# Optimization experiments

Measured on AMD Instinct MI355X. Metric: run time of the kernel, lower is better.

## Reference

```python
import jax, jax.numpy as jnp
import numpy as np

C = 256
NH, NL, NP_ = 8, 3, 4
HD = C // NH
NLAYERS = 6


def sine_pos(H, W, num_feats=128, temperature=10000.0, eps=1e-6):
    # mmdet SinePositionalEncoding with normalize=True and an all-zero padding mask:
    # cumsum of ones -> (i+1), normalized by last element (H or W) * 2*pi.
    scale = 2.0 * np.pi
    y = (jnp.arange(1, H + 1, dtype=jnp.float32) / (H + eps)) * scale
    x = (jnp.arange(1, W + 1, dtype=jnp.float32) / (W + eps)) * scale
    d = jnp.arange(num_feats, dtype=jnp.float32)
    dim_t = temperature ** (2.0 * jnp.floor(d / 2.0) / num_feats)

    def interleave(p):  # p: (n, num_feats) -> sin on even dims, cos on odd dims, interleaved
        return jnp.stack([jnp.sin(p[:, 0::2]), jnp.cos(p[:, 1::2])], axis=-1).reshape(p.shape[0], -1)

    py = interleave(y[:, None] / dim_t)  # (H, num_feats)
    px = interleave(x[:, None] / dim_t)  # (W, num_feats)
    pos = jnp.concatenate([jnp.broadcast_to(py[:, None, :], (H, W, num_feats)),
                           jnp.broadcast_to(px[None, :, :], (H, W, num_feats))], axis=-1)
    return pos.reshape(H * W, 2 * num_feats)


def ref_points(H, W):
    # normalized pixel centers, (x, y) order, shape (H*W, 2)
    ry = (jnp.arange(H, dtype=jnp.float32) + 0.5) / H
    rx = (jnp.arange(W, dtype=jnp.float32) + 0.5) / W
    gy, gx = jnp.meshgrid(ry, rx, indexing='ij')
    return jnp.stack([gx.ravel(), gy.ravel()], axis=-1)


def ln(x, w, b, eps=1e-5):
    m = x.mean(-1, keepdims=True)
    v = x.var(-1, keepdims=True)
    return (x - m) / jnp.sqrt(v + eps) * w + b


def gnorm(x, w, b, groups=32, eps=1e-5):
    B, Ch, H, W = x.shape
    xg = x.reshape(B, groups, Ch // groups, H, W)
    m = xg.mean((2, 3, 4), keepdims=True)
    v = xg.var((2, 3, 4), keepdims=True)
    xg = (xg - m) / jnp.sqrt(v + eps)
    return xg.reshape(B, Ch, H, W) * w[None, :, None, None] + b[None, :, None, None]


def conv3x3(x, w):
    return jax.lax.conv_general_dilated(x, w, (1, 1), 'SAME',
                                        dimension_numbers=('NCHW', 'OIHW', 'NCHW'))


def ms_deform(value, shapes, loc, aw):
    # value (B,S,NH,HD); loc (B,L,NH,NL,NP,2) normalized [0,1]; aw (B,L,NH,NL,NP)
    # Matches F.grid_sample(..., align_corners=False, padding_mode='zeros').
    B, S, nH, hd = value.shape
    Lq, nP = loc.shape[1], loc.shape[4]
    out = jnp.zeros((B, Lq, nH, hd), value.dtype)
    start = 0
    for lvl, (H, W) in enumerate(shapes):
        v = value[:, start:start + H * W].transpose(0, 2, 1, 3)  # (B,nH,HW,hd)
        start += H * W
        l = loc[:, :, :, lvl]                 # (B,Lq,nH,nP,2)
        px = l[..., 0] * W - 0.5
        py = l[..., 1] * H - 0.5
        x0 = jnp.floor(px); y0 = jnp.floor(py)
        lx = px - x0; ly = py - y0
        x0i = x0.astype(jnp.int32); y0i = y0.astype(jnp.int32)

        def tw(w_):  # (B,Lq,nH,nP) -> (B,nH,Lq*nP,1)
            return w_.transpose(0, 2, 1, 3).reshape(B, nH, Lq * nP, 1)

        def gather(xi, yi):
            valid = ((xi >= 0) & (xi < W) & (yi >= 0) & (yi < H)).astype(value.dtype)
            idx = jnp.clip(yi, 0, H - 1) * W + jnp.clip(xi, 0, W - 1)
            idx = idx.transpose(0, 2, 1, 3).reshape(B, nH, Lq * nP)
            g = jnp.take_along_axis(v, idx[..., None], axis=2)  # (B,nH,Lq*nP,hd)
            return g * tw(valid)

        samp = (gather(x0i, y0i) * tw((1 - lx) * (1 - ly))
                + gather(x0i + 1, y0i) * tw(lx * (1 - ly))
                + gather(x0i, y0i + 1) * tw((1 - lx) * ly)
                + gather(x0i + 1, y0i + 1) * tw(lx * ly))
        samp = samp.reshape(B, nH, Lq, nP, hd)
        out = out + jnp.einsum('bqhp,bhqpd->bqhd', aw[:, :, :, lvl], samp)
    return out.reshape(B, Lq, nH * hd)


def _forward(feat0, feat1, feat2, in0_w, in0_b, in1_w, in1_b, in2_w, in2_b,
             off_w, off_b, aw_w, aw_b, vp_w, vp_b, op_w, op_b,
             n1_w, n1_b, ff1_w, ff1_b, ff2_w, ff2_b, n2_w, n2_b,
             fn_w, fn_b, lat_w, lat_b, out_w, gnw, gnb):
    feats = [feat0, feat1, feat2]
    in_ws = [in0_w, in1_w, in2_w]; in_bs = [in0_b, in1_b, in2_b]
    B = feat0.shape[0]
    mlvl = [jnp.einsum('oi,bihw->bohw', w, f) + b[None, :, None, None]
            for f, w, b in zip(feats, in_ws, in_bs)]
    shapes = [(f.shape[2], f.shape[3]) for f in mlvl]
    src = jnp.concatenate([f.reshape(B, C, -1).transpose(0, 2, 1) for f in mlvl], axis=1)  # (B,L,C)
    pos = jnp.concatenate([sine_pos(H, W) for (H, W) in shapes], axis=0)[None]  # (1,L,C)
    ref = jnp.concatenate([ref_points(H, W) for (H, W) in shapes], axis=0)      # (L,2)
    L = ref.shape[0]
    ref = jnp.broadcast_to(ref[None, :, None, :], (B, L, NL, 2))
    norm = jnp.array([[w_, h_] for (h_, w_) in shapes], dtype=src.dtype)  # (NL,2) = (W,H)
    for i in range(NLAYERS):
        q = src + pos
        off = (q @ off_w[i].T + off_b[i]).reshape(B, L, NH, NL, NP_, 2)
        aw = jax.nn.softmax((q @ aw_w[i].T + aw_b[i]).reshape(B, L, NH, NL * NP_), axis=-1)
        aw = aw.reshape(B, L, NH, NL, NP_)
        value = (src @ vp_w[i].T + vp_b[i]).reshape(B, L, NH, HD)
        loc = ref[:, :, None, :, None, :] + off / norm[None, None, None, :, None, :]
        attn = ms_deform(value, shapes, loc, aw) @ op_w[i].T + op_b[i]
        src = ln(src + attn, n1_w[i], n1_b[i])
        ff = jax.nn.relu(src @ ff1_w[i].T + ff1_b[i]) @ ff2_w[i].T + ff2_b[i]
        src = ln(src + ff, n2_w[i], n2_b[i])
    src = ln(src, fn_w, fn_b)
    mems, s = [], 0
    for (H, W) in shapes:
        mems.append(src[:, s:s + H * W].transpose(0, 2, 1).reshape(B, C, H, W))
        s += H * W
    mf = jnp.einsum('oi,bihw->bohw', lat_w, mems[0]) + lat_b[None, :, None, None]
    for i in range(3):
        mf = jax.nn.relu(gnorm(conv3x3(mf, out_w[i]), gnw[i], gnb[i]))
    return (mf, mems[0], mems[1], mems[2])


def setup_inputs():
    ks = iter(jax.random.split(jax.random.key(0), 64))

    def rn(shape, s=0.02):
        return jax.random.normal(next(ks), shape, dtype=jnp.float32) * s

    return dict(
        feat0=rn((1, 256, 64, 64), 1.0),
        feat1=rn((1, 512, 32, 32), 1.0),
        feat2=rn((1, 1024, 16, 16), 1.0),
        in0_w=rn((256, 256)), in0_b=rn((256,)),
        in1_w=rn((256, 512)), in1_b=rn((256,)),
        in2_w=rn((256, 1024)), in2_b=rn((256,)),
        off_w=rn((6, 192, 256), 0.002), off_b=rn((6, 192), 0.5),
        aw_w=rn((6, 96, 256)), aw_b=jnp.zeros((6, 96), jnp.float32),
        vp_w=rn((6, 256, 256)), vp_b=rn((6, 256)),
        op_w=rn((6, 256, 256)), op_b=rn((6, 256)),
        n1_w=jnp.ones((6, 256), jnp.float32), n1_b=jnp.zeros((6, 256), jnp.float32),
        ff1_w=rn((6, 1024, 256)), ff1_b=rn((6, 1024)),
        ff2_w=rn((6, 256, 1024)), ff2_b=rn((6, 256)),
        n2_w=jnp.ones((6, 256), jnp.float32), n2_b=jnp.zeros((6, 256), jnp.float32),
        fn_w=jnp.ones((256,), jnp.float32), fn_b=jnp.zeros((256,), jnp.float32),
        lat_w=rn((256, 256)), lat_b=rn((256,)),
        out_w=rn((3, 256, 256, 3, 3)),
        gnw=jnp.ones((3, 256), jnp.float32), gnb=jnp.zeros((3, 256), jnp.float32),
    )


def reference(feat0, feat1, feat2, in0_w, in0_b, in1_w, in1_b, in2_w, in2_b,
              off_w, off_b, aw_w, aw_b, vp_w, vp_b, op_w, op_b,
              n1_w, n1_b, ff1_w, ff1_b, ff2_w, ff2_b, n2_w, n2_b,
              fn_w, fn_b, lat_w, lat_b, out_w, gnw, gnb):
    return _forward(feat0, feat1, feat2, in0_w, in0_b, in1_w, in1_b, in2_w, in2_b,
                    off_w, off_b, aw_w, aw_b, vp_w, vp_b, op_w, op_b,
                    n1_w, n1_b, ff1_w, ff1_b, ff2_w, ff2_b, n2_w, n2_b,
                    fn_w, fn_b, lat_w, lat_b, out_w, gnw, gnb)
```

## Files before the change

kernel.cpp:

```cpp
#include <hip/hip_runtime.h>
#include <math.h>

#define LTOT 5376

typedef __attribute__((ext_vector_type(8))) __bf16 bf16x8;
typedef __attribute__((ext_vector_type(4))) float f32x4;
typedef __attribute__((ext_vector_type(8))) unsigned short us8;
typedef __attribute__((ext_vector_type(4))) unsigned short us4;

static __device__ __forceinline__ float4 ld4(const float* p) { return *(const float4*)p; }

static __device__ __forceinline__ unsigned short f2bf(float f) {
    unsigned int u = __float_as_uint(f);
    return (unsigned short)((u + 0x7fffu + ((u >> 16) & 1u)) >> 16);
}
static __device__ __forceinline__ float bf2f(unsigned short s) {
    return __uint_as_float(((unsigned int)s) << 16);
}

static __device__ __forceinline__ void gl16(const unsigned short* g, unsigned short* l) {
    __builtin_amdgcn_global_load_lds(
        (const __attribute__((address_space(1))) unsigned int*)g,
        (__attribute__((address_space(3))) unsigned int*)l, 16, 0, 0);
}

__device__ __forceinline__ void gemm_core(
    const unsigned short* __restrict__ A,
    const unsigned short* __restrict__ B,
    const float* __restrict__ bias,
    float* __restrict__ C1, unsigned short* __restrict__ C2,
    const float* __restrict__ posf, unsigned short* __restrict__ qb,
    unsigned short* As, unsigned short* Bs,
    int m0, int mo0, int n0, int N, int K, int omode, int relu)
{
    const int tid  = threadIdx.x;
    const int wave = tid >> 6;
    const int lane = tid & 63;
    const int wm   = (wave >> 1) * 32;
    const int wn   = (wave & 1) * 32;
    const int fr   = lane & 15;
    const int ko   = lane >> 4;

    const int q0 = tid, q1 = tid + 256;
    const int r0 = q0 >> 3, c0v = (q0 & 7) ^ (r0 & 7);
    const int r1 = q1 >> 3, c1v = (q1 & 7) ^ (r1 & 7);
    const unsigned short* a0 = A + (size_t)(m0 + r0) * K + (c0v << 3);
    const unsigned short* a1 = A + (size_t)(m0 + r1) * K + (c1v << 3);
    int bn0 = n0 + r0; if (bn0 > N - 1) bn0 = N - 1;
    int bn1 = n0 + r1; if (bn1 > N - 1) bn1 = N - 1;
    const unsigned short* b0 = B + (size_t)bn0 * K + (c0v << 3);
    const unsigned short* b1 = B + (size_t)bn1 * K + (c1v << 3);
    const int wb = wave << 9;

    f32x4 acc[2][2] = {};
    const int nt = K >> 6;

    auto stage = [&](int buf, int t) {
        const int kof = t << 6;
        gl16(a0 + kof, As + buf * 4096 + wb);
        gl16(a1 + kof, As + buf * 4096 + 2048 + wb);
        gl16(b0 + kof, Bs + buf * 4096 + wb);
        gl16(b1 + kof, Bs + buf * 4096 + 2048 + wb);
    };

    stage(0, 0);
    stage(1, 1);
    asm volatile("s_waitcnt vmcnt(4)" ::: "memory");
    __builtin_amdgcn_s_barrier();
    __builtin_amdgcn_sched_barrier(0);

    for (int t = 0; t < nt; t++) {
        if (t + 2 < nt) stage((t + 2) % 3, t + 2);
        const unsigned short* Ab = As + (t % 3) * 4096;
        const unsigned short* Bb = Bs + (t % 3) * 4096;
        #pragma unroll
        for (int sub = 0; sub < 2; sub++) {
            bf16x8 af[2], bfr[2];
            const int kk = (sub << 2) + ko;
            #pragma unroll
            for (int i = 0; i < 2; i++) {
                int r = wm + i * 16 + fr;
                af[i] = *(const bf16x8*)&Ab[(r << 6) + ((kk ^ (r & 7)) << 3)];
                int c = wn + i * 16 + fr;
                bfr[i] = *(const bf16x8*)&Bb[(c << 6) + ((kk ^ (c & 7)) << 3)];
            }
            #pragma unroll
            for (int i = 0; i < 2; i++)
                #pragma unroll
                for (int j = 0; j < 2; j++)
                    acc[i][j] = __builtin_amdgcn_mfma_f32_16x16x32_bf16(af[i], bfr[j], acc[i][j], 0, 0, 0);
        }
        if (t + 1 < nt) {
            if (t + 2 < nt) asm volatile("s_waitcnt vmcnt(4) lgkmcnt(0)" ::: "memory");
            else            asm volatile("s_waitcnt vmcnt(0) lgkmcnt(0)" ::: "memory");
            __builtin_amdgcn_s_barrier();
            __builtin_amdgcn_sched_barrier(0);
        }
    }

    #pragma unroll
    for (int j = 0; j < 2; j++) {
        int col = n0 + wn + j * 16 + fr;
        if (col >= N) continue;
        float cb = bias[col];
        #pragma unroll
        for (int i = 0; i < 2; i++) {
            #pragma unroll
            for (int r = 0; r < 4; r++) {
                int row = mo0 + wm + i * 16 + ko * 4 + r;
                float v = acc[i][j][r] + cb;
                if (relu) v = fmaxf(v, 0.f);
                size_t off = (size_t)row * N + col;
                if (omode == 0)      C1[off] = v;
                else if (omode == 1) C2[off] = f2bf(v);
                else if (omode == 2) { C1[off] = v; C2[off] = f2bf(v); }
                else { C1[off] = v; C2[off] = f2bf(v); qb[off] = f2bf(v + posf[off]); }
            }
        }
    }
}

__global__ __launch_bounds__(256) void bgemm_k(
    const unsigned short* __restrict__ A, const unsigned short* __restrict__ B,
    const float* __restrict__ bias, float* __restrict__ C1, unsigned short* __restrict__ C2,
    int N, int K, int omode, int relu)
{
    __shared__ unsigned short As[3 * 4096], Bs[3 * 4096];
    int m = blockIdx.y * 64;
    gemm_core(A, B, bias, C1, C2, nullptr, nullptr, As, Bs, m, m, blockIdx.x * 64, N, K, omode, relu);
}

__global__ __launch_bounds__(256) void oavp_k(
    const unsigned short* __restrict__ qbb, const unsigned short* __restrict__ woa,
    const float* __restrict__ boa, float* __restrict__ oab,
    const unsigned short* __restrict__ srcb, const unsigned short* __restrict__ wvp,
    const float* __restrict__ bvp, unsigned short* __restrict__ valb)
{
    __shared__ unsigned short As[3 * 4096], Bs[3 * 4096];
    const int bx = blockIdx.x;
    const int m = blockIdx.y * 64;
    if (bx < 5)
        gemm_core(qbb,  woa, boa, oab, nullptr, nullptr, nullptr, As, Bs, m, m, bx * 64, 288, 256, 0, 0);
    else
        gemm_core(srcb, wvp, bvp, nullptr, valb, nullptr, nullptr, As, Bs, m, m, (bx - 5) * 64, 256, 256, 1, 0);
}

__global__ __launch_bounds__(256) void inproj_k(
    const unsigned short* __restrict__ fT0, const unsigned short* __restrict__ w0, const float* __restrict__ b0,
    const unsigned short* __restrict__ fT1, const unsigned short* __restrict__ w1, const float* __restrict__ b1,
    const unsigned short* __restrict__ fT2, const unsigned short* __restrict__ w2, const float* __restrict__ b2,
    float* __restrict__ src, unsigned short* __restrict__ srcb,
    const float* __restrict__ posf, unsigned short* __restrict__ qbb)
{
    __shared__ unsigned short As[3 * 4096], Bs[3 * 4096];
    const int by = blockIdx.y;
    const int n0 = blockIdx.x * 64;
    if (by < 64)
        gemm_core(fT0, w0, b0, src, srcb, posf, qbb, As, Bs, by * 64, by * 64, n0, 256, 256, 3, 0);
    else if (by < 80)
        gemm_core(fT1, w1, b1, src, srcb, posf, qbb, As, Bs, (by - 64) * 64, 4096 + (by - 64) * 64, n0, 256, 512, 3, 0);
    else
        gemm_core(fT2, w2, b2, src, srcb, posf, qbb, As, Bs, (by - 80) * 64, 5120 + (by - 80) * 64, n0, 256, 1024, 3, 0);
}

__global__ __launch_bounds__(256) void setup_k(
    const float* __restrict__ off_w, const float* __restrict__ off_b,
    const float* __restrict__ aw_w,  const float* __restrict__ aw_b,
    unsigned short* __restrict__ w_oa, float* __restrict__ b_oa,
    const float* __restrict__ out_w, unsigned short* __restrict__ wcb,
    const float* __restrict__ s0, const float* __restrict__ s1,
    const float* __restrict__ s2, const float* __restrict__ s3,
    const float* __restrict__ s4, const float* __restrict__ s5,
    const float* __restrict__ s6, const float* __restrict__ s7,
    unsigned short* __restrict__ dcvt,
    float* __restrict__ pos,
    const float* __restrict__ f0, const float* __restrict__ f1, const float* __restrict__ f2,
    unsigned short* __restrict__ d0, unsigned short* __restrict__ d1, unsigned short* __restrict__ d2)
{
    const int bid = blockIdx.x;
    const int tid = threadIdx.x;
    if (bid < 1728) {
        int idx = bid * 256 + tid;
        int i = idx / 73728;
        int r = idx - i * 73728;
        int n = r >> 8;
        int k = r & 255;
        float v = (n < 192) ? off_w[((size_t)i * 192 + n) * 256 + k]
                            : aw_w[((size_t)i * 96 + (n - 192)) * 256 + k];
        w_oa[idx] = f2bf(v);
        if (k == 0)
            b_oa[i * 288 + n] = (n < 192) ? off_b[i * 192 + n] : aw_b[i * 96 + (n - 192)];
    } else if (bid < 8640) {
        int idx = (bid - 1728) * 256 + tid;
        int c   = idx / 589824;
        int r   = idx - c * 589824;
        int icc = r / 73728;
        int r2  = r - icc * 73728;
        int oc  = r2 / 288;
        int r3  = r2 - oc * 288;
        int tap = r3 >> 5;
        int sl  = r3 & 31;
        int ic  = icc * 32 + (((sl >> 3) ^ ((oc >> 1) & 3)) << 3) + (sl & 7);
        wcb[idx] = f2bf(out_w[(((size_t)(c * 256 + oc)) * 256 + ic) * 9 + tap]);
    } else if (bid < 12992) {
        int i = (bid - 8640) * 256 + tid;
        const float* s; int off;
        if      (i <   98304) { s = s0; off = 0; }
        else if (i <  196608) { s = s1; off = 98304; }
        else if (i <  589824) { s = s2; off = 196608; }
        else if (i <  983040) { s = s3; off = 589824; }
        else if (i <  999424) { s = s4; off = 983040; }
        else if (i < 1032192) { s = s5; off = 999424; }
        else if (i < 1097728) { s = s6; off = 1032192; }
        else                  { s = s7; off = 1097728; }
        float4 v = ld4(&s[(size_t)(i - off) << 2]);
        us4 r = { f2bf(v.x), f2bf(v.y), f2bf(v.z), f2bf(v.w) };
        *(us4*)&dcvt[(size_t)i << 2] = r;
    } else if (bid < 15680) {
        int idx = (bid - 12992) * 256 + tid;
        int l = idx >> 7;
        int pr = idx & 127;
        int half = pr >> 6;
        int j = pr & 63;
        int HW, sh, p;
        if (l < 4096)      { HW = 64; sh = 6; p = l; }
        else if (l < 5120) { HW = 32; sh = 5; p = l - 4096; }
        else               { HW = 16; sh = 4; p = l - 5120; }
        int y = p >> sh;
        int x = p & (HW - 1);
        float invT = exp2f((float)j * (-13.287712379549449f / 64.f));
        float coord = (half == 0) ? (float)(y + 1) : (float)(x + 1);
        float v = coord / ((float)HW + 1e-6f) * 6.283185307179586f;
        float arg = v * invT;
        size_t base = (size_t)l * 256 + half * 128 + (j << 1);
        pos[base]     = sinf(arg);
        pos[base + 1] = cosf(arg);
    } else {
        __shared__ float t[32][33];
        int b = bid - 15680;
        const float* src; unsigned short* dst; int Ci, P, bx, by;
        if (b < 1024)      { src = f0; dst = d0; Ci = 256;  P = 4096; bx = b & 127;        by = b >> 7; }
        else if (b < 1536) { src = f1; dst = d1; Ci = 512;  P = 1024; bx = (b - 1024) & 31; by = (b - 1024) >> 5; }
        else               { src = f2; dst = d2; Ci = 1024; P = 256;  bx = (b - 1536) & 7;  by = (b - 1536) >> 3; }
        int c0 = by * 32, p0 = bx * 32;
        int x = tid & 31, y = tid >> 5;
        for (int i = y; i < 32; i += 8)
            t[i][x] = src[(size_t)(c0 + i) * P + p0 + x];
        __syncthreads();
        for (int i = y; i < 32; i += 8)
            dst[(size_t)(p0 + i) * Ci + c0 + x] = f2bf(t[x][i]);
    }
}

__global__ __launch_bounds__(256) void msdef_k(
    const unsigned short* __restrict__ valb, const float* __restrict__ oab,
    unsigned short* __restrict__ out)
{
    __shared__ float sw[8 * 288];
    const int tid = threadIdx.x;
    const int bl = blockIdx.x;
    #pragma unroll
    for (int id = tid; id < 576; id += 256)
        ((float4*)sw)[id] = ((const float4*)(oab + (size_t)bl * 2304))[id];
    __syncthreads();

    const int p = tid >> 5;
    const int t = tid & 31;
    const int l = bl * 8 + p;
    const int h = t >> 2;
    const int co = (t & 3) << 3;
    const float* mo = sw + p * 288;

    float aw_r[12];
    {
        const float* sc = mo + 192 + h * 12;
        float mx = -1e30f;
        #pragma unroll
        for (int j = 0; j < 12; j++) { aw_r[j] = sc[j]; mx = fmaxf(mx, aw_r[j]); }
        float su = 0.f;
        #pragma unroll
        for (int j = 0; j < 12; j++) { aw_r[j] = expf(aw_r[j] - mx); su += aw_r[j]; }
        float inv = 1.f / su;
        #pragma unroll
        for (int j = 0; j < 12; j++) aw_r[j] *= inv;
    }

    float rx, ry;
    {
        int HW, sh, q;
        if (l < 4096)      { HW = 64; sh = 6; q = l; }
        else if (l < 5120) { HW = 32; sh = 5; q = l - 4096; }
        else               { HW = 16; sh = 4; q = l - 5120; }
        int y = q >> sh;
        int x = q & (HW - 1);
        rx = (x + 0.5f) / (float)HW;
        ry = (y + 0.5f) / (float)HW;
    }

    const int starts[3] = {0, 4096, 5120};
    const int dims[3]   = {64, 32, 16};
    float acc[8] = {};
    #pragma unroll
    for (int s = 0; s < 3; s++) {
        const int D = dims[s];
        const int st = starts[s];
        #pragma unroll
        for (int pt = 0; pt < 4; pt++) {
            float a  = aw_r[(s << 2) + pt];
            float px = rx * D + mo[h * 24 + (s << 3) + (pt << 1)]     - 0.5f;
            float py = ry * D + mo[h * 24 + (s << 3) + (pt << 1) + 1] - 0.5f;
            float x0f = floorf(px), y0f = floorf(py);
            float lx = px - x0f, ly = py - y0f;
            int x0 = (int)x0f, y0 = (int)y0f;
            float w00 = a * (1.f - lx) * (1.f - ly);
            float w10 = a * lx * (1.f - ly);
            float w01 = a * (1.f - lx) * ly;
            float w11 = a * lx * ly;
            #pragma unroll
            for (int cy = 0; cy < 2; cy++) {
                int yi = y0 + cy;
                if (yi < 0 || yi >= D) continue;
                #pragma unroll
                for (int cx = 0; cx < 2; cx++) {
                    int xi = x0 + cx;
                    if (xi < 0 || xi >= D) continue;
                    float w = cy ? (cx ? w11 : w01) : (cx ? w10 : w00);
                    us8 v = *(const us8*)&valb[((size_t)(st + yi * D + xi) << 8) + (h << 5) + co];
                    #pragma unroll
                    for (int e = 0; e < 8; e++)
                        acc[e] = fmaf(w, bf2f(v[e]), acc[e]);
                }
            }
        }
    }
    us8 r;
    #pragma unroll
    for (int e = 0; e < 8; e++) r[e] = f2bf(acc[e]);
    *(us8*)&out[((size_t)l << 8) + (h << 5) + co] = r;
}

template<bool HAS_POS>
__global__ __launch_bounds__(256) void ln_k(float* __restrict__ src, const float* __restrict__ add,
                                            const float* __restrict__ w, const float* __restrict__ b,
                                            unsigned short* __restrict__ outb,
                                            const float* __restrict__ posf,
                                            unsigned short* __restrict__ qbout)
{
    int row = blockIdx.x * 4 + (threadIdx.x >> 6);
    int lane = threadIdx.x & 63;
    size_t base = (size_t)row * 256 + (lane << 2);
    float4 x = ld4(&src[base]);
    float4 a = ld4(&add[base]);
    x.x += a.x; x.y += a.y; x.z += a.z; x.w += a.w;
    float s = x.x + x.y + x.z + x.w;
    #pragma unroll
    for (int o = 32; o > 0; o >>= 1) s += __shfl_xor(s, o, 64);
    float m = s * (1.f / 256.f);
    float d0 = x.x - m, d1 = x.y - m, d2 = x.z - m, d3 = x.w - m;
    float v = d0 * d0 + d1 * d1 + d2 * d2 + d3 * d3;
    #pragma unroll
    for (int o = 32; o > 0; o >>= 1) v += __shfl_xor(v, o, 64);
    float rs = rsqrtf(v * (1.f / 256.f) + 1e-5f);
    float4 wv = ld4(&w[lane << 2]);
    float4 bv = ld4(&b[lane << 2]);
    float4 o4;
    o4.x = d0 * rs * wv.x + bv.x;
    o4.y = d1 * rs * wv.y + bv.y;
    o4.z = d2 * rs * wv.z + bv.z;
    o4.w = d3 * rs * wv.w + bv.w;
    *(float4*)&src[base] = o4;
    us4 r = { f2bf(o4.x), f2bf(o4.y), f2bf(o4.z), f2bf(o4.w) };
    *(us4*)&outb[base] = r;
    if (HAS_POS) {
        float4 p4 = ld4(&posf[base]);
        us4 q = { f2bf(o4.x + p4.x), f2bf(o4.y + p4.y), f2bf(o4.z + p4.z), f2bf(o4.w + p4.w) };
        *(us4*)&qbout[base] = q;
    }
}

__global__ __launch_bounds__(256) void ln2fn_k(float* __restrict__ src, const float* __restrict__ add,
                                               const float* __restrict__ w2, const float* __restrict__ b2,
                                               const float* __restrict__ wf, const float* __restrict__ bf,
                                               unsigned short* __restrict__ outb)
{
    int row = blockIdx.x * 4 + (threadIdx.x >> 6);
    int lane = threadIdx.x & 63;
    size_t base = (size_t)row * 256 + (lane << 2);
    float4 x = ld4(&src[base]);
    float4 a = ld4(&add[base]);
    x.x += a.x; x.y += a.y; x.z += a.z; x.w += a.w;
    float s = x.x + x.y + x.z + x.w;
    #pragma unroll
    for (int o = 32; o > 0; o >>= 1) s += __shfl_xor(s, o, 64);
    float m = s * (1.f / 256.f);
    float d0 = x.x - m, d1 = x.y - m, d2 = x.z - m, d3 = x.w - m;
    float v = d0 * d0 + d1 * d1 + d2 * d2 + d3 * d3;
    #pragma unroll
    for (int o = 32; o > 0; o >>= 1) v += __shfl_xor(v, o, 64);
    float rs = rsqrtf(v * (1.f / 256.f) + 1e-5f);
    float4 wv = ld4(&w2[lane << 2]);
    float4 bv = ld4(&b2[lane << 2]);
    float4 o4;
    o4.x = d0 * rs * wv.x + bv.x;
    o4.y = d1 * rs * wv.y + bv.y;
    o4.z = d2 * rs * wv.z + bv.z;
    o4.w = d3 * rs * wv.w + bv.w;
    float s2 = o4.x + o4.y + o4.z + o4.w;
    #pragma unroll
    for (int o = 32; o > 0; o >>= 1) s2 += __shfl_xor(s2, o, 64);
    float m2 = s2 * (1.f / 256.f);
    float e0 = o4.x - m2, e1 = o4.y - m2, e2 = o4.z - m2, e3 = o4.w - m2;
    float v2 = e0 * e0 + e1 * e1 + e2 * e2 + e3 * e3;
    #pragma unroll
    for (int o = 32; o > 0; o >>= 1) v2 += __shfl_xor(v2, o, 64);
    float rs2 = rsqrtf(v2 * (1.f / 256.f) + 1e-5f);
    float4 wf4 = ld4(&wf[lane << 2]);
    float4 bf4 = ld4(&bf[lane << 2]);
    float4 o5;
    o5.x = e0 * rs2 * wf4.x + bf4.x;
    o5.y = e1 * rs2 * wf4.y + bf4.y;
    o5.z = e2 * rs2 * wf4.z + bf4.z;
    o5.w = e3 * rs2 * wf4.w + bf4.w;
    *(float4*)&src[base] = o5;
    us4 r = { f2bf(o5.x), f2bf(o5.y), f2bf(o5.z), f2bf(o5.w) };
    *(us4*)&outb[base] = r;
}

__global__ __launch_bounds__(256) void tail_k(
    const float* __restrict__ src, float* __restrict__ outb_,
    const unsigned short* __restrict__ srcb, const unsigned short* __restrict__ w_lat,
    const float* __restrict__ lat_b, unsigned short* __restrict__ latb)
{
    if (blockIdx.x < 1344) {
        __shared__ float t[32][33];
        int b = blockIdx.x;
        int bx = b % 168, cy = b / 168;
        const float* s; float* d; int HW, p0;
        if (bx < 128)      { s = src;           d = outb_;           HW = 4096; p0 = bx * 32; }
        else if (bx < 160) { s = src + 1048576; d = outb_ + 1048576; HW = 1024; p0 = (bx - 128) * 32; }
        else               { s = src + 1310720; d = outb_ + 1310720; HW = 256;  p0 = (bx - 160) * 32; }
        int c0 = cy * 32;
        int x = threadIdx.x & 31, y = threadIdx.x >> 5;
        for (int i = y; i < 32; i += 8)
            t[i][x] = s[(size_t)(p0 + i) * 256 + c0 + x];
        __syncthreads();
        for (int i = y; i < 32; i += 8)
            d[(size_t)(c0 + i) * HW + p0 + x] = t[x][i];
    } else {
        __shared__ unsigned short As[3 * 4096], Bs[3 * 4096];
        int b = blockIdx.x - 1344;
        int m = (b >> 2) * 64;
        gemm_core(srcb, w_lat, lat_b, nullptr, latb, nullptr, nullptr, As, Bs,
                  m, m, (b & 3) * 64, 256, 256, 1, 0);
    }
}

__global__ __launch_bounds__(256) void conv3b_k(const unsigned short* __restrict__ inb,
                                                const unsigned short* __restrict__ wcb,
                                                float* __restrict__ out)
{
    __shared__ __align__(16) unsigned char smem[25344];
    unsigned short* sIn = (unsigned short*)smem;
    unsigned short* sW  = (unsigned short*)(smem + 6912);
    float* sO = (float*)smem;

    const int tid = threadIdx.x;
    const int mb = blockIdx.x;
    const int y0 = (mb >> 2) << 2;
    const int x0 = (mb & 3) << 4;
    const int oc0 = blockIdx.y << 5;
    const int wave = tid >> 6, lane = tid & 63;
    const int wm = (wave >> 1) * 32;
    const int wn = (wave & 1) * 16;
    const int fr = lane & 15, ko = lane >> 4;

    f32x4 acc[2] = {};

    for (int icc = 0; icc < 8; icc++) {
        __syncthreads();
        #pragma unroll
        for (int id = tid; id < 432; id += 256) {
            int pxi = id >> 2, ch = id & 3;
            int r = pxi / 18, s = pxi - r * 18;
            int gy = y0 - 1 + r, gx = x0 - 1 + s;
            us8 v = {};
            if (gy >= 0 && gy < 64 && gx >= 0 && gx < 64)
                v = *(const us8*)&inb[((size_t)(gy * 64 + gx) << 8) + (icc << 5) + (ch << 3)];
            *(us8*)&sIn[(pxi << 5) + ((ch ^ ((s >> 1) & 3)) << 3)] = v;
        }
        const unsigned short* wsrc = wcb + (((size_t)icc * 256 + oc0) * 9 << 5);
        #pragma unroll
        for (int id = tid; id < 1152; id += 256)
            *(us8*)&sW[id << 3] = *(const us8*)&wsrc[id << 3];
        __syncthreads();

        #pragma unroll
        for (int tap = 0; tap < 9; tap++) {
            const int ky = tap / 3, kx = tap - ky * 3;
            bf16x8 a[2], b;
            #pragma unroll
            for (int i = 0; i < 2; i++) {
                int px = wm + i * 16 + fr;
                int r = (px >> 4) + ky;
                int s = (px & 15) + kx;
                a[i] = *(const bf16x8*)&sIn[(((r * 18 + s)) << 5) + ((ko ^ ((s >> 1) & 3)) << 3)];
            }
            {
                int oc = wn + fr;
                b = *(const bf16x8*)&sW[(((oc * 9) + tap) << 5) + ((ko ^ ((oc >> 1) & 3)) << 3)];
            }
            #pragma unroll
            for (int i = 0; i < 2; i++)
                acc[i] = __builtin_amdgcn_mfma_f32_16x16x32_bf16(a[i], b, acc[i], 0, 0, 0);
        }
    }

    __syncthreads();
    #pragma unroll
    for (int i = 0; i < 2; i++) {
        int oc = wn + fr;
        int pxb = wm + i * 16 + ko * 4;
        *(f32x4*)&sO[oc * 68 + pxb] = acc[i];
    }
    __syncthreads();
    {
        int oc_r = tid >> 3;
        int yy   = (tid >> 1) & 3;
        int xh   = (tid & 1) << 3;
        float* dst = &out[(size_t)(oc0 + oc_r) * 4096 + (y0 + yy) * 64 + x0 + xh];
        const float* srcl = &sO[oc_r * 68 + yy * 16 + xh];
        *(float4*)&dst[0] = *(const float4*)&srcl[0];
        *(float4*)&dst[4] = *(const float4*)&srcl[4];
    }
}

template<int OUT>
__global__ __launch_bounds__(1024) void gn_k(const float* __restrict__ x,
                                             const float* __restrict__ w, const float* __restrict__ b,
                                             unsigned short* __restrict__ ob, float* __restrict__ of)
{
    const int g = blockIdx.x;
    const float* p = x + (size_t)g * 32768;
    float s = 0.f, ss = 0.f;
    for (int i = threadIdx.x * 4; i < 32768; i += 4096) {
        float4 v = ld4(&p[i]);
        s  += v.x + v.y + v.z + v.w;
        ss += v.x * v.x + v.y * v.y + v.z * v.z + v.w * v.w;
    }
    #pragma unroll
    for (int o = 32; o > 0; o >>= 1) {
        s  += __shfl_xor(s, o, 64);
        ss += __shfl_xor(ss, o, 64);
    }
    __shared__ float rs[16], rss[16];
    int wid = threadIdx.x >> 6;
    if ((threadIdx.x & 63) == 0) { rs[wid] = s; rss[wid] = ss; }
    __syncthreads();
    float S = 0.f, SS = 0.f;
    #pragma unroll
    for (int k = 0; k < 16; k++) { S += rs[k]; SS += rss[k]; }
    float m = S * (1.f / 32768.f);
    float rstd = rsqrtf(SS * (1.f / 32768.f) - m * m + 1e-5f);

    for (int i = threadIdx.x; i < 8192; i += 1024) {
        int cl = i >> 10;
        int c = (g << 3) + cl;
        float sw = w[c], sb = b[c];
        float4 v = ld4(&p[(size_t)i << 2]);
        float r0 = fmaxf((v.x - m) * rstd * sw + sb, 0.f);
        float r1 = fmaxf((v.y - m) * rstd * sw + sb, 0.f);
        float r2 = fmaxf((v.z - m) * rstd * sw + sb, 0.f);
        float r3 = fmaxf((v.w - m) * rstd * sw + sb, 0.f);
        if (OUT == 0) {
            int px0 = (i & 1023) << 2;
            ob[(size_t)(px0 + 0) * 256 + c] = f2bf(r0);
            ob[(size_t)(px0 + 1) * 256 + c] = f2bf(r1);
            ob[(size_t)(px0 + 2) * 256 + c] = f2bf(r2);
            ob[(size_t)(px0 + 3) * 256 + c] = f2bf(r3);
        } else {
            float4 r = make_float4(r0, r1, r2, r3);
            *(float4*)&of[(size_t)g * 32768 + ((size_t)i << 2)] = r;
        }
    }
}

extern "C" void kernel_launch(void* const* d_in, const int* in_sizes, int n_in,
                              void* d_out, int out_size, void* d_ws, size_t ws_size,
                              hipStream_t stream)
{
    (void)in_sizes; (void)n_in; (void)out_size; (void)ws_size;
    const float* feat0 = (const float*)d_in[0];
    const float* feat1 = (const float*)d_in[1];
    const float* feat2 = (const float*)d_in[2];
    const float* in0_w = (const float*)d_in[3];
    const float* in0_b = (const float*)d_in[4];
    const float* in1_w = (const float*)d_in[5];
    const float* in1_b = (const float*)d_in[6];
    const float* in2_w = (const float*)d_in[7];
    const float* in2_b = (const float*)d_in[8];
    const float* off_w = (const float*)d_in[9];
    const float* off_b = (const float*)d_in[10];
    const float* aw_w  = (const float*)d_in[11];
    const float* aw_b  = (const float*)d_in[12];
    const float* vp_w  = (const float*)d_in[13];
    const float* vp_b  = (const float*)d_in[14];
    const float* op_w  = (const float*)d_in[15];
    const float* op_b  = (const float*)d_in[16];
    const float* n1_w  = (const float*)d_in[17];
    const float* n1_b  = (const float*)d_in[18];
    const float* ff1_w = (const float*)d_in[19];
    const float* ff1_b = (const float*)d_in[20];
    const float* ff2_w = (const float*)d_in[21];
    const float* ff2_b = (const float*)d_in[22];
    const float* n2_w  = (const float*)d_in[23];
    const float* n2_b  = (const float*)d_in[24];
    const float* fn_w  = (const float*)d_in[25];
    const float* fn_b  = (const float*)d_in[26];
    const float* lat_w = (const float*)d_in[27];
    const float* lat_b = (const float*)d_in[28];
    const float* out_w = (const float*)d_in[29];
    const float* gnw   = (const float*)d_in[30];
    const float* gnb   = (const float*)d_in[31];
    float* out = (float*)d_out;

    float* ws     = (float*)d_ws;
    float* src    = ws;
    float* pos    = src  + 1376256;
    float* tmp    = pos  + 1376256;
    float* valbuf = tmp  + 1376256;
    float* oab    = valbuf + 1376256;
    float* stats  = oab  + 1548288;
    float* boa    = stats + 64;
    float* pong   = pos;

    unsigned short* valb = (unsigned short*)valbuf;
    unsigned short* latb = (unsigned short*)(valbuf + 688128);

    unsigned short* ub = (unsigned short*)(boa + 1728);
    unsigned short* srcb  = ub; ub += 1376256;
    unsigned short* qbb   = ub; ub += 1376256;
    unsigned short* msdb  = ub; ub += 1376256;
    unsigned short* ffhb  = ub; ub += 5505024;
    unsigned short* w_oa  = ub; ub += 442368;
    unsigned short* w_vp  = ub; ub += 393216;
    unsigned short* w_op  = ub; ub += 393216;
    unsigned short* w_ff1 = ub; ub += 1572864;
    unsigned short* w_ff2 = ub; ub += 1572864;
    unsigned short* w_in0 = ub; ub += 65536;
    unsigned short* w_in1 = ub; ub += 131072;
    unsigned short* w_in2 = ub; ub += 262144;
    unsigned short* w_lat = ub; ub += 65536;
    unsigned short* wcb   = ub; ub += 1769472;

    unsigned short* fT0 = ffhb;
    unsigned short* fT1 = ffhb + 1048576;
    unsigned short* fT2 = ffhb + 1572864;
    unsigned short* pingb = qbb;

    setup_k<<<17472, 256, 0, stream>>>(off_w, off_b, aw_w, aw_b, w_oa, boa,
                                       out_w, wcb,
                                       vp_w, op_w, ff1_w, ff2_w, in0_w, in1_w, in2_w, lat_w, w_vp,
                                       pos,
                                       feat0, feat1, feat2, fT0, fT1, fT2);

    inproj_k<<<dim3(4, 84), 256, 0, stream>>>(fT0, w_in0, in0_b, fT1, w_in1, in1_b,
                                              fT2, w_in2, in2_b, src, srcb, pos, qbb);

    for (int i = 0; i < 6; i++) {
        oavp_k<<<dim3(9, 84), 256, 0, stream>>>(qbb, w_oa + i*73728, boa + i*288, oab,
                                                srcb, w_vp + i*65536, vp_b + i*256, valb);
        msdef_k<<<672, 256, 0, stream>>>(valb, oab, msdb);
        bgemm_k<<<dim3(4, 84), 256, 0, stream>>>(msdb, w_op + i*65536, op_b + i*256, tmp, nullptr, 256, 256, 0, 0);
        ln_k<false><<<1344, 256, 0, stream>>>(src, tmp, n1_w + i*256, n1_b + i*256, srcb, nullptr, nullptr);
        bgemm_k<<<dim3(16, 84), 256, 0, stream>>>(srcb, w_ff1 + i*262144, ff1_b + i*1024, nullptr, ffhb, 1024, 256, 1, 1);
        bgemm_k<<<dim3(4, 84), 256, 0, stream>>>(ffhb, w_ff2 + i*262144, ff2_b + i*256, tmp, nullptr, 256, 1024, 0, 0);
        if (i < 5)
            ln_k<true><<<1344, 256, 0, stream>>>(src, tmp, n2_w + i*256, n2_b + i*256, srcb, pos, qbb);
        else
            ln2fn_k<<<1344, 256, 0, stream>>>(src, tmp, n2_w + i*256, n2_b + i*256, fn_w, fn_b, srcb);
    }

    tail_k<<<1600, 256, 0, stream>>>(src, out + 1048576, srcb, w_lat, lat_b, latb);

    conv3b_k<<<dim3(64, 8), 256, 0, stream>>>(latb, wcb, pong);
    gn_k<0><<<32, 1024, 0, stream>>>(pong, gnw, gnb, pingb, nullptr);

    conv3b_k<<<dim3(64, 8), 256, 0, stream>>>(pingb, wcb + 589824, pong);
    gn_k<0><<<32, 1024, 0, stream>>>(pong, gnw + 256, gnb + 256, pingb, nullptr);

    conv3b_k<<<dim3(64, 8), 256, 0, stream>>>(pingb, wcb + 1179648, pong);
    gn_k<1><<<32, 1024, 0, stream>>>(pong, gnw + 512, gnb + 512, nullptr, out);
}
```

Measured before the change: 606.0 us.

## Split-K the N=256 GEMMs and 3x3 convs, reducing partials in consumers

Adds a split-K GEMM kernel that runs the output-projection and FFN2 GEMMs as two K halves. The second half uses a zero bias and writes a separate partial buffer, and the LayerNorm kernels add that partial. The 3x3 conv kernels likewise split the input-channel loop across grid.z into two output buffers, which GroupNorm sums while loading. The aim is to double the block count on these under-occupied 336/512-block launches, in exchange for extra partial-buffer memory traffic.

```diff
diff --git a/kernel.cpp b/kernel.cpp
--- a/kernel.cpp
+++ b/kernel.cpp
@@ -31,7 +31,7 @@
     float* __restrict__ C1, unsigned short* __restrict__ C2,
     const float* __restrict__ posf, unsigned short* __restrict__ qb,
     unsigned short* As, unsigned short* Bs,
-    int m0, int mo0, int n0, int N, int K, int omode, int relu)
+    int m0, int mo0, int n0, int N, int Kloop, int ldk, int omode, int relu)
 {
     const int tid  = threadIdx.x;
     const int wave = tid >> 6;
@@ -44,16 +44,16 @@
     const int q0 = tid, q1 = tid + 256;
     const int r0 = q0 >> 3, c0v = (q0 & 7) ^ (r0 & 7);
     const int r1 = q1 >> 3, c1v = (q1 & 7) ^ (r1 & 7);
-    const unsigned short* a0 = A + (size_t)(m0 + r0) * K + (c0v << 3);
-    const unsigned short* a1 = A + (size_t)(m0 + r1) * K + (c1v << 3);
+    const unsigned short* a0 = A + (size_t)(m0 + r0) * ldk + (c0v << 3);
+    const unsigned short* a1 = A + (size_t)(m0 + r1) * ldk + (c1v << 3);
     int bn0 = n0 + r0; if (bn0 > N - 1) bn0 = N - 1;
     int bn1 = n0 + r1; if (bn1 > N - 1) bn1 = N - 1;
-    const unsigned short* b0 = B + (size_t)bn0 * K + (c0v << 3);
-    const unsigned short* b1 = B + (size_t)bn1 * K + (c1v << 3);
+    const unsigned short* b0 = B + (size_t)bn0 * ldk + (c0v << 3);
+    const unsigned short* b1 = B + (size_t)bn1 * ldk + (c1v << 3);
     const int wb = wave << 9;
 
     f32x4 acc[2][2] = {};
-    const int nt = K >> 6;
+    const int nt = Kloop >> 6;
 
     auto stage = [&](int buf, int t) {
         const int kof = t << 6;
@@ -127,7 +127,21 @@
 {
     __shared__ unsigned short As[3 * 4096], Bs[3 * 4096];
     int m = blockIdx.y * 64;
-    gemm_core(A, B, bias, C1, C2, nullptr, nullptr, As, Bs, m, m, blockIdx.x * 64, N, K, omode, relu);
+    gemm_core(A, B, bias, C1, C2, nullptr, nullptr, As, Bs, m, m, blockIdx.x * 64, N, K, K, omode, relu);
+}
+
+__global__ __launch_bounds__(256) void bgemmsk_k(
+    const unsigned short* __restrict__ A, const unsigned short* __restrict__ B,
+    const float* __restrict__ bias, const float* __restrict__ zbuf,
+    float* __restrict__ C0, float* __restrict__ C1p, int N, int fullK)
+{
+    __shared__ unsigned short As[3 * 4096], Bs[3 * 4096];
+    const int m = blockIdx.y * 64;
+    const int kp = blockIdx.z;
+    const int Ks = fullK >> 1;
+    gemm_core(A + kp * Ks, B + kp * Ks, kp ? zbuf : bias,
+              kp ? C1p : C0, nullptr, nullptr, nullptr,
+              As, Bs, m, m, blockIdx.x * 64, N, Ks, fullK, 0, 0);
 }
 
 __global__ __launch_bounds__(256) void oavp_k(
@@ -140,9 +154,9 @@
     const int bx = blockIdx.x;
     const int m = blockIdx.y * 64;
     if (bx < 5)
-        gemm_core(qbb,  woa, boa, oab, nullptr, nullptr, nullptr, As, Bs, m, m, bx * 64, 288, 256, 0, 0);
+        gemm_core(qbb,  woa, boa, oab, nullptr, nullptr, nullptr, As, Bs, m, m, bx * 64, 288, 256, 256, 0, 0);
     else
-        gemm_core(srcb, wvp, bvp, nullptr, valb, nullptr, nullptr, As, Bs, m, m, (bx - 5) * 64, 256, 256, 1, 0);
+        gemm_core(srcb, wvp, bvp, nullptr, valb, nullptr, nullptr, As, Bs, m, m, (bx - 5) * 64, 256, 256, 256, 1, 0);
 }
 
 __global__ __launch_bounds__(256) void inproj_k(
@@ -156,11 +170,11 @@
     const int by = blockIdx.y;
     const int n0 = blockIdx.x * 64;
     if (by < 64)
-        gemm_core(fT0, w0, b0, src, srcb, posf, qbb, As, Bs, by * 64, by * 64, n0, 256, 256, 3, 0);
+        gemm_core(fT0, w0, b0, src, srcb, posf, qbb, As, Bs, by * 64, by * 64, n0, 256, 256, 256, 3, 0);
     else if (by < 80)
-        gemm_core(fT1, w1, b1, src, srcb, posf, qbb, As, Bs, (by - 64) * 64, 4096 + (by - 64) * 64, n0, 256, 512, 3, 0);
+        gemm_core(fT1, w1, b1, src, srcb, posf, qbb, As, Bs, (by - 64) * 64, 4096 + (by - 64) * 64, n0, 256, 512, 512, 3, 0);
     else
-        gemm_core(fT2, w2, b2, src, srcb, posf, qbb, As, Bs, (by - 80) * 64, 5120 + (by - 80) * 64, n0, 256, 1024, 3, 0);
+        gemm_core(fT2, w2, b2, src, srcb, posf, qbb, As, Bs, (by - 80) * 64, 5120 + (by - 80) * 64, n0, 256, 1024, 1024, 3, 0);
 }
 
 __global__ __launch_bounds__(256) void setup_k(
@@ -175,7 +189,8 @@
     unsigned short* __restrict__ dcvt,
     float* __restrict__ pos,
     const float* __restrict__ f0, const float* __restrict__ f1, const float* __restrict__ f2,
-    unsigned short* __restrict__ d0, unsigned short* __restrict__ d1, unsigned short* __restrict__ d2)
+    unsigned short* __restrict__ d0, unsigned short* __restrict__ d1, unsigned short* __restrict__ d2,
+    float* __restrict__ zbuf)
 {
     const int bid = blockIdx.x;
     const int tid = threadIdx.x;
@@ -190,6 +205,7 @@
         w_oa[idx] = f2bf(v);
         if (k == 0)
             b_oa[i * 288 + n] = (n < 192) ? off_b[i * 192 + n] : aw_b[i * 96 + (n - 192)];
+        if (bid == 0) zbuf[tid] = 0.f;
     } else if (bid < 8640) {
         int idx = (bid - 1728) * 256 + tid;
         int c   = idx / 589824;
@@ -341,6 +357,7 @@
 
 template<bool HAS_POS>
 __global__ __launch_bounds__(256) void ln_k(float* __restrict__ src, const float* __restrict__ add,
+                                            const float* __restrict__ add2,
                                             const float* __restrict__ w, const float* __restrict__ b,
                                             unsigned short* __restrict__ outb,
                                             const float* __restrict__ posf,
@@ -351,7 +368,8 @@
     size_t base = (size_t)row * 256 + (lane << 2);
     float4 x = ld4(&src[base]);
     float4 a = ld4(&add[base]);
-    x.x += a.x; x.y += a.y; x.z += a.z; x.w += a.w;
+    float4 a2 = ld4(&add2[base]);
+    x.x += a.x + a2.x; x.y += a.y + a2.y; x.z += a.z + a2.z; x.w += a.w + a2.w;
     float s = x.x + x.y + x.z + x.w;
     #pragma unroll
     for (int o = 32; o > 0; o >>= 1) s += __shfl_xor(s, o, 64);
@@ -379,6 +397,7 @@
 }
 
 __global__ __launch_bounds__(256) void ln2fn_k(float* __restrict__ src, const float* __restrict__ add,
+                                               const float* __restrict__ add2,
                                                const float* __restrict__ w2, const float* __restrict__ b2,
                                                const float* __restrict__ wf, const float* __restrict__ bf,
                                                unsigned short* __restrict__ outb)
@@ -388,7 +407,8 @@
     size_t base = (size_t)row * 256 + (lane << 2);
     float4 x = ld4(&src[base]);
     float4 a = ld4(&add[base]);
-    x.x += a.x; x.y += a.y; x.z += a.z; x.w += a.w;
+    float4 a2 = ld4(&add2[base]);
+    x.x += a.x + a2.x; x.y += a.y + a2.y; x.z += a.z + a2.z; x.w += a.w + a2.w;
     float s = x.x + x.y + x.z + x.w;
     #pragma unroll
     for (int o = 32; o > 0; o >>= 1) s += __shfl_xor(s, o, 64);
@@ -451,13 +471,14 @@
         int b = blockIdx.x - 1344;
         int m = (b >> 2) * 64;
         gemm_core(srcb, w_lat, lat_b, nullptr, latb, nullptr, nullptr, As, Bs,
-                  m, m, (b & 3) * 64, 256, 256, 1, 0);
+                  m, m, (b & 3) * 64, 256, 256, 256, 1, 0);
     }
 }
 
 __global__ __launch_bounds__(256) void conv3b_k(const unsigned short* __restrict__ inb,
                                                 const unsigned short* __restrict__ wcb,
-                                                float* __restrict__ out)
+                                                float* __restrict__ out0,
+                                                float* __restrict__ out1)
 {
     __shared__ __align__(16) unsigned char smem[25344];
     unsigned short* sIn = (unsigned short*)smem;
@@ -469,6 +490,8 @@
     const int y0 = (mb >> 2) << 2;
     const int x0 = (mb & 3) << 4;
     const int oc0 = blockIdx.y << 5;
+    const int icc0 = blockIdx.z << 2;
+    float* out = blockIdx.z ? out1 : out0;
     const int wave = tid >> 6, lane = tid & 63;
     const int wm = (wave >> 1) * 32;
     const int wn = (wave & 1) * 16;
@@ -476,7 +499,7 @@
 
     f32x4 acc[2] = {};
 
-    for (int icc = 0; icc < 8; icc++) {
+    for (int icc = icc0; icc < icc0 + 4; icc++) {
         __syncthreads();
         #pragma unroll
         for (int id = tid; id < 432; id += 256) {
@@ -535,17 +558,20 @@
 }
 
 template<int OUT>
-__global__ __launch_bounds__(1024) void gn_k(const float* __restrict__ x,
+__global__ __launch_bounds__(1024) void gn_k(const float* __restrict__ x0, const float* __restrict__ x1,
                                              const float* __restrict__ w, const float* __restrict__ b,
                                              unsigned short* __restrict__ ob, float* __restrict__ of)
 {
     const int g = blockIdx.x;
-    const float* p = x + (size_t)g * 32768;
+    const float* p0 = x0 + (size_t)g * 32768;
+    const float* p1 = x1 + (size_t)g * 32768;
     float s = 0.f, ss = 0.f;
     for (int i = threadIdx.x * 4; i < 32768; i += 4096) {
-        float4 v = ld4(&p[i]);
-        s  += v.x + v.y + v.z + v.w;
-        ss += v.x * v.x + v.y * v.y + v.z * v.z + v.w * v.w;
+        float4 v0 = ld4(&p0[i]);
+        float4 v1 = ld4(&p1[i]);
+        float e0 = v0.x + v1.x, e1 = v0.y + v1.y, e2 = v0.z + v1.z, e3 = v0.w + v1.w;
+        s  += e0 + e1 + e2 + e3;
+        ss += e0 * e0 + e1 * e1 + e2 * e2 + e3 * e3;
     }
     #pragma unroll
     for (int o = 32; o > 0; o >>= 1) {
@@ -566,11 +592,12 @@
         int cl = i >> 10;
         int c = (g << 3) + cl;
         float sw = w[c], sb = b[c];
-        float4 v = ld4(&p[(size_t)i << 2]);
-        float r0 = fmaxf((v.x - m) * rstd * sw + sb, 0.f);
-        float r1 = fmaxf((v.y - m) * rstd * sw + sb, 0.f);
-        float r2 = fmaxf((v.z - m) * rstd * sw + sb, 0.f);
-        float r3 = fmaxf((v.w - m) * rstd * sw + sb, 0.f);
+        float4 v0 = ld4(&p0[(size_t)i << 2]);
+        float4 v1 = ld4(&p1[(size_t)i << 2]);
+        float r0 = fmaxf((v0.x + v1.x - m) * rstd * sw + sb, 0.f);
+        float r1 = fmaxf((v0.y + v1.y - m) * rstd * sw + sb, 0.f);
+        float r2 = fmaxf((v0.z + v1.z - m) * rstd * sw + sb, 0.f);
+        float r3 = fmaxf((v0.w + v1.w - m) * rstd * sw + sb, 0.f);
         if (OUT == 0) {
             int px0 = (i & 1023) << 2;
             ob[(size_t)(px0 + 0) * 256 + c] = f2bf(r0);
@@ -631,12 +658,15 @@
     float* oab    = valbuf + 1376256;
     float* stats  = oab  + 1548288;
     float* boa    = stats + 64;
+    float* zbuf   = boa  + 1728;
+    float* tmp2   = zbuf + 256;
     float* pong   = pos;
+    float* pong2  = tmp;
 
     unsigned short* valb = (unsigned short*)valbuf;
     unsigned short* latb = (unsigned short*)(valbuf + 688128);
 
-    unsigned short* ub = (unsigned short*)(boa + 1728);
+    unsigned short* ub = (unsigned short*)(tmp2 + 1376256);
     unsigned short* srcb  = ub; ub += 1376256;
     unsigned short* qbb   = ub; ub += 1376256;
     unsigned short* msdb  = ub; ub += 1376256;
@@ -661,7 +691,7 @@
                                        out_w, wcb,
                                        vp_w, op_w, ff1_w, ff2_w, in0_w, in1_w, in2_w, lat_w, w_vp,
                                        pos,
-                                       feat0, feat1, feat2, fT0, fT1, fT2);
+                                       feat0, feat1, feat2, fT0, fT1, fT2, zbuf);
 
     inproj_k<<<dim3(4, 84), 256, 0, stream>>>(fT0, w_in0, in0_b, fT1, w_in1, in1_b,
                                               fT2, w_in2, in2_b, src, srcb, pos, qbb);
@@ -670,24 +700,30 @@
         oavp_k<<<dim3(9, 84), 256, 0, stream>>>(qbb, w_oa + i*73728, boa + i*288, oab,
                                                 srcb, w_vp + i*65536, vp_b + i*256, valb);
         msdef_k<<<672, 256, 0, stream>>>(valb, oab, msdb);
-        bgemm_k<<<dim3(4, 84), 256, 0, stream>>>(msdb, w_op + i*65536, op_b + i*256, tmp, nullptr, 256, 256, 0, 0);
-        ln_k<false><<<1344, 256, 0, stream>>>(src, tmp, n1_w + i*256, n1_b + i*256, srcb, nullptr, nullptr);
-        bgemm_k<<<dim3(16, 84), 256, 0, stream>>>(srcb, w_ff1 + i*262144, ff1_b + i*1024, nullptr, ffhb, 1024, 256, 1, 1);
-        bgemm_k<<<dim3(4, 84), 256, 0, stream>>>(ffhb, w_ff2 + i*262144, ff2_b + i*256, tmp, nullptr, 256, 1024, 0, 0);
+        bgemmsk_k<<<dim3(4, 84, 2), 256, 0, stream>>>(msdb, w_op + i*65536, op_b + i*256, zbuf,
+                                                      tmp, tmp2, 256, 256);
+        ln_k<false><<<1344, 256, 0, stream>>>(src, tmp, tmp2, n1_w + i*256, n1_b + i*256,
+                                              srcb, nullptr, nullptr);
+        bgemm_k<<<dim3(16, 84), 256, 0, stream>>>(srcb, w_ff1 + i*262144, ff1_b + i*1024,
+                                                  nullptr, ffhb, 1024, 256, 1, 1);
+        bgemmsk_k<<<dim3(4, 84, 2), 256, 0, stream>>>(ffhb, w_ff2 + i*262144, ff2_b + i*256, zbuf,
+                                                      tmp, tmp2, 256, 1024);
         if (i < 5)
-            ln_k<true><<<1344, 256, 0, stream>>>(src, tmp, n2_w + i*256, n2_b + i*256, srcb, pos, qbb);
+            ln_k<true><<<1344, 256, 0, stream>>>(src, tmp, tmp2, n2_w + i*256, n2_b + i*256,
+                                                 srcb, pos, qbb);
         else
-            ln2fn_k<<<1344, 256, 0, stream>>>(src, tmp, n2_w + i*256, n2_b + i*256, fn_w, fn_b, srcb);
+            ln2fn_k<<<1344, 256, 0, stream>>>(src, tmp, tmp2, n2_w + i*256, n2_b + i*256,
+                                              fn_w, fn_b, srcb);
     }
 
     tail_k<<<1600, 256, 0, stream>>>(src, out + 1048576, srcb, w_lat, lat_b, latb);
 
-    conv3b_k<<<dim3(64, 8), 256, 0, stream>>>(latb, wcb, pong);
-    gn_k<0><<<32, 1024, 0, stream>>>(pong, gnw, gnb, pingb, nullptr);
-
-    conv3b_k<<<dim3(64, 8), 256, 0, stream>>>(pingb, wcb + 589824, pong);
-    gn_k<0><<<32, 1024, 0, stream>>>(pong, gnw + 256, gnb + 256, pingb, nullptr);
-
-    conv3b_k<<<dim3(64, 8), 256, 0, stream>>>(pingb, wcb + 1179648, pong);
-    gn_k<1><<<32, 1024, 0, stream>>>(pong, gnw + 512, gnb + 512, nullptr, out);
-}
+    conv3b_k<<<dim3(64, 8, 2), 256, 0, stream>>>(latb, wcb, pong, pong2);
+    gn_k<0><<<32, 1024, 0, stream>>>(pong, pong2, gnw, gnb, pingb, nullptr);
+
+    conv3b_k<<<dim3(64, 8, 2), 256, 0, stream>>>(pingb, wcb + 589824, pong, pong2);
+    gn_k<0><<<32, 1024, 0, stream>>>(pong, pong2, gnw + 256, gnb + 256, pingb, nullptr);
+
+    conv3b_k<<<dim3(64, 8, 2), 256, 0, stream>>>(pingb, wcb + 1179648, pong, pong2);
+    gn_k<1><<<32, 1024, 0, stream>>>(pong, pong2, gnw + 512, gnb + 512, nullptr, out);
+}
```

Measured after the change: 571.7 us. 1.06x faster.
